# Kernel optimization log

Hardware: AMD Instinct MI355X
Metric: run time of the kernel (lower is better)

The kernel has to match this reference:

```python
import jax, jax.numpy as jnp
import numpy as np

EPS = 1e-5  # nn.GroupNorm default


def setup_inputs() -> dict:
    key = jax.random.key(0)
    k1, k2, k3 = jax.random.split(key, 3)
    N, B, C, H, W = 8, 4, 256, 64, 64
    blocks = jax.random.normal(k1, (N, B, C, H, W), dtype=jnp.float32)
    x = jax.random.normal(k2, (B, C, H, W), dtype=jnp.float32)
    w = jax.random.normal(k3, (C,), dtype=jnp.float32) * 0.02
    gn_weight = jnp.ones((C,), dtype=jnp.float32)
    gn_bias = jnp.zeros((C,), dtype=jnp.float32)
    return {"blocks": blocks, "x": x, "w": w, "gn_weight": gn_weight, "gn_bias": gn_bias}


def reference(blocks, x, w, gn_weight, gn_bias):
    # V: [N1, B, C, H, W] = prior blocks + current features
    V = jnp.concatenate([blocks, x[None]], axis=0)
    # GroupNorm(1, C): normalize over (C, H, W) per (n, b) sample, per-channel affine
    mean = jnp.mean(V, axis=(2, 3, 4), keepdims=True)
    var = jnp.var(V, axis=(2, 3, 4), keepdims=True)
    K = (V - mean) * jax.lax.rsqrt(var + EPS)
    K = K * gn_weight[None, None, :, None, None] + gn_bias[None, None, :, None, None]
    # channel-dim dot product -> logits over depth blocks
    logits = jnp.einsum('c,nbchw->nbhw', w, K)
    attn = jax.nn.softmax(logits, axis=0)  # softmax over depth-block axis N1
    h = jnp.einsum('nbhw,nbchw->bchw', attn, V)
    return h
```

## Files before the change

### kernel.cpp

```cpp
#include <hip/hip_runtime.h>


#define NPRI 8
#define N1   9
#define BB   4
#define CC   256
#define HWN  4096
#define CHW  (CC * HWN)
#define NB   (N1 * BB)
#define GN_EPS 1e-5f

#define WS_PSUM   0
#define WS_PSQ    2304
#define WS_SPART  4608
#define WS_ATTN   594432

__global__ __launch_bounds__(256, 4) void k1_stats(
        const float* __restrict__ blocks, const float* __restrict__ x,
        const float* __restrict__ w, const float* __restrict__ gnw,
        float* __restrict__ ws) {
    const int bid   = blockIdx.x;
    const int nb    = bid >> 6;
    const int rem   = bid & 63;
    const int cq    = rem >> 4;
    const int hwseg = rem & 15;
    const int t     = threadIdx.x;
    const int cg    = t >> 6;
    const int lane  = t & 63;

    const float* base = (nb < NPRI * BB)
        ? blocks + (size_t)nb * CHW
        : x + (size_t)(nb - NPRI * BB) * CHW;

    const int hw0 = hwseg * 256 + lane * 4;
    const int c0  = cq * 64 + cg * 16;

    float s0 = 0.f, s1 = 0.f, s2 = 0.f, s3 = 0.f;
    float sum = 0.f, sq = 0.f;

    #pragma unroll 4
    for (int c = c0; c < c0 + 16; ++c) {
        const float4 v = *reinterpret_cast<const float4*>(base + (size_t)c * HWN + hw0);
        const float wg = w[c] * gnw[c];
        sum += v.x + v.y + v.z + v.w;
        sq  += v.x * v.x + v.y * v.y + v.z * v.z + v.w * v.w;
        s0 += wg * v.x; s1 += wg * v.y; s2 += wg * v.z; s3 += wg * v.w;
    }

    __shared__ float4 sbuf[3][64];
    if (cg) sbuf[cg - 1][lane] = make_float4(s0, s1, s2, s3);
    __syncthreads();
    if (!cg) {
        #pragma unroll
        for (int g = 0; g < 3; ++g) {
            const float4 o = sbuf[g][lane];
            s0 += o.x; s1 += o.y; s2 += o.z; s3 += o.w;
        }
        float* Sp = ws + WS_SPART;
        *reinterpret_cast<float4*>(Sp + (size_t)(cq * NB + nb) * HWN + hw0) =
            make_float4(s0, s1, s2, s3);
    }

    #pragma unroll
    for (int off = 32; off; off >>= 1) {
        sum += __shfl_down(sum, off);
        sq  += __shfl_down(sq, off);
    }
    __shared__ float red[8];
    if (lane == 0) { red[cg] = sum; red[4 + cg] = sq; }
    __syncthreads();
    if (t == 0) {
        const int slot = nb * 64 + rem;
        ws[WS_PSUM + slot] = red[0] + red[1] + red[2] + red[3];
        ws[WS_PSQ  + slot] = red[4] + red[5] + red[6] + red[7];
    }
}

__global__ __launch_bounds__(256) void k2_attn(
        const float* __restrict__ w, const float* __restrict__ gnw,
        const float* __restrict__ gnb, float* __restrict__ ws) {
    const int t = threadIdx.x;

    __shared__ float red[8];
    __shared__ float swg_s, swgb_s;
    __shared__ float mean_s[NB], rstd_s[NB];

    float p = w[t] * gnw[t];
    float q = w[t] * gnb[t];
    #pragma unroll
    for (int off = 32; off; off >>= 1) {
        p += __shfl_down(p, off);
        q += __shfl_down(q, off);
    }
    const int wave = t >> 6, lane = t & 63;
    if (lane == 0) { red[wave] = p; red[4 + wave] = q; }

    if (t < NB) {
        float s = 0.f, ss = 0.f;
        #pragma unroll 8
        for (int i = 0; i < 64; ++i) {
            s  += ws[WS_PSUM + t * 64 + i];
            ss += ws[WS_PSQ  + t * 64 + i];
        }
        const float mean = s * (1.0f / CHW);
        const float var  = ss * (1.0f / CHW) - mean * mean;
        mean_s[t] = mean;
        rstd_s[t] = rsqrtf(var + GN_EPS);
    }
    __syncthreads();
    if (t == 0) {
        swg_s  = red[0] + red[1] + red[2] + red[3];
        swgb_s = red[4] + red[5] + red[6] + red[7];
    }
    __syncthreads();
    const float swg = swg_s, swgb = swgb_s;

    const int idx = blockIdx.x * 256 + t;
    const int b  = idx >> 12;
    const int hw = idx & 4095;

    const float* Sp = ws + WS_SPART;
    float* attn = ws + WS_ATTN;

    float logit[N1];
    float mx = -1e30f;
    #pragma unroll
    for (int n = 0; n < N1; ++n) {
        const int nb = n * BB + b;
        const size_t o = (size_t)nb * HWN + hw;
        const float S = Sp[o] + Sp[(size_t)NB * HWN + o]
                      + Sp[(size_t)2 * NB * HWN + o] + Sp[(size_t)3 * NB * HWN + o];
        const float l = rstd_s[nb] * (S - mean_s[nb] * swg) + swgb;
        logit[n] = l;
        mx = fmaxf(mx, l);
    }
    float denom = 0.f;
    #pragma unroll
    for (int n = 0; n < N1; ++n) {
        const float e = __expf(logit[n] - mx);
        logit[n] = e;
        denom += e;
    }
    const float inv = 1.0f / denom;
    #pragma unroll
    for (int n = 0; n < N1; ++n)
        attn[(size_t)(n * BB + b) * HWN + hw] = logit[n] * inv;
}

__global__ __launch_bounds__(256) void k3_out(
        const float* __restrict__ blocks, const float* __restrict__ x,
        const float* __restrict__ ws, float* __restrict__ out) {
    const int bid = blockIdx.x;
    const int hwq = bid & 3;
    const int c   = (bid >> 2) & (CC - 1);
    const int b   = bid >> 10;
    const int t   = threadIdx.x;
    const int hw0 = hwq * 1024 + t * 4;

    const float* attn = ws + WS_ATTN;
    float a0 = 0.f, a1 = 0.f, a2 = 0.f, a3 = 0.f;

    #pragma unroll
    for (int n = 0; n < N1; ++n) {
        const float* vbase = (n < NPRI)
            ? blocks + ((size_t)(n * BB + b) * CC + c) * HWN
            : x + ((size_t)b * CC + c) * HWN;
        const float4 v = *reinterpret_cast<const float4*>(vbase + hw0);
        const float4 a = *reinterpret_cast<const float4*>(
            attn + (size_t)(n * BB + b) * HWN + hw0);
        a0 += a.x * v.x; a1 += a.y * v.y; a2 += a.z * v.z; a3 += a.w * v.w;
    }
    float* optr = out + ((size_t)(b * CC + c)) * HWN + hw0;
    __builtin_nontemporal_store(a0, optr + 0);
    __builtin_nontemporal_store(a1, optr + 1);
    __builtin_nontemporal_store(a2, optr + 2);
    __builtin_nontemporal_store(a3, optr + 3);
}

extern "C" void kernel_launch(void* const* d_in, const int* in_sizes, int n_in,
                              void* d_out, int out_size, void* d_ws, size_t ws_size,
                              hipStream_t stream) {
    const float* blocks = (const float*)d_in[0];
    const float* x      = (const float*)d_in[1];
    const float* w      = (const float*)d_in[2];
    const float* gnw    = (const float*)d_in[3];
    const float* gnb    = (const float*)d_in[4];
    float* out = (float*)d_out;
    float* ws  = (float*)d_ws;

    hipLaunchKernelGGL(k1_stats, dim3(2304), dim3(256), 0, stream, blocks, x, w, gnw, ws);
    hipLaunchKernelGGL(k2_attn, dim3(64), dim3(256), 0, stream, w, gnw, gnb, ws);
    hipLaunchKernelGGL(k3_out, dim3(4096), dim3(256), 0, stream, blocks, x, ws, out);
}
```

Baseline: 59.42 us.

## Fuse softmax attention computation into output weighted-sum kernel

```diff
diff --git a/kernel.cpp b/kernel.cpp
--- a/kernel.cpp
+++ b/kernel.cpp
@@ -13,7 +13,6 @@
 #define WS_PSUM   0
 #define WS_PSQ    2304
 #define WS_SPART  4608
-#define WS_ATTN   594432
 
 __global__ __launch_bounds__(256, 4) void k1_stats(
         const float* __restrict__ blocks, const float* __restrict__ x,
@@ -76,24 +75,33 @@
     }
 }
 
-__global__ __launch_bounds__(256) void k2_attn(
+__global__ __launch_bounds__(256, 4) void k2_fused(
+        const float* __restrict__ blocks, const float* __restrict__ x,
         const float* __restrict__ w, const float* __restrict__ gnw,
-        const float* __restrict__ gnb, float* __restrict__ ws) {
-    const int t = threadIdx.x;
+        const float* __restrict__ gnb,
+        const float* __restrict__ ws, float* __restrict__ out) {
+    const int bid = blockIdx.x;
+    const int b   = bid >> 9;
+    const int hw0 = (bid & 511) * 8;
+    const int t   = threadIdx.x;
 
     __shared__ float red[8];
     __shared__ float swg_s, swgb_s;
     __shared__ float mean_s[NB], rstd_s[NB];
+    __shared__ float logit_s[N1][8];
+    __shared__ float4 attn4_s[N1][2];
 
-    float p = w[t] * gnw[t];
-    float q = w[t] * gnb[t];
-    #pragma unroll
-    for (int off = 32; off; off >>= 1) {
-        p += __shfl_down(p, off);
-        q += __shfl_down(q, off);
+    {
+        float p = w[t] * gnw[t];
+        float q = w[t] * gnb[t];
+        #pragma unroll
+        for (int off = 32; off; off >>= 1) {
+            p += __shfl_down(p, off);
+            q += __shfl_down(q, off);
+        }
+        const int wave = t >> 6, lane = t & 63;
+        if (lane == 0) { red[wave] = p; red[4 + wave] = q; }
     }
-    const int wave = t >> 6, lane = t & 63;
-    if (lane == 0) { red[wave] = p; red[4 + wave] = q; }
 
     if (t < NB) {
         float s = 0.f, ss = 0.f;
@@ -113,68 +121,63 @@
         swgb_s = red[4] + red[5] + red[6] + red[7];
     }
     __syncthreads();
-    const float swg = swg_s, swgb = swgb_s;
 
-    const int idx = blockIdx.x * 256 + t;
-    const int b  = idx >> 12;
-    const int hw = idx & 4095;
-
-    const float* Sp = ws + WS_SPART;
-    float* attn = ws + WS_ATTN;
-
-    float logit[N1];
-    float mx = -1e30f;
-    #pragma unroll
-    for (int n = 0; n < N1; ++n) {
-        const int nb = n * BB + b;
-        const size_t o = (size_t)nb * HWN + hw;
+    if (t < N1 * 8) {
+        const int n   = t >> 3;
+        const int hwi = t & 7;
+        const int nb  = n * BB + b;
+        const float* Sp = ws + WS_SPART;
+        const size_t o = (size_t)nb * HWN + hw0 + hwi;
         const float S = Sp[o] + Sp[(size_t)NB * HWN + o]
                       + Sp[(size_t)2 * NB * HWN + o] + Sp[(size_t)3 * NB * HWN + o];
-        const float l = rstd_s[nb] * (S - mean_s[nb] * swg) + swgb;
-        logit[n] = l;
-        mx = fmaxf(mx, l);
+        logit_s[n][hwi] = rstd_s[nb] * (S - mean_s[nb] * swg_s) + swgb_s;
     }
-    float denom = 0.f;
-    #pragma unroll
-    for (int n = 0; n < N1; ++n) {
-        const float e = __expf(logit[n] - mx);
-        logit[n] = e;
-        denom += e;
+    __syncthreads();
+
+    if (t < 8) {
+        float mx = -1e30f;
+        #pragma unroll
+        for (int n = 0; n < N1; ++n) mx = fmaxf(mx, logit_s[n][t]);
+        float den = 0.f;
+        float e[N1];
+        #pragma unroll
+        for (int n = 0; n < N1; ++n) { e[n] = __expf(logit_s[n][t] - mx); den += e[n]; }
+        const float inv = 1.0f / den;
+        float* attn_f = (float*)attn4_s;
+        #pragma unroll
+        for (int n = 0; n < N1; ++n) attn_f[n * 8 + t] = e[n] * inv;
     }
-    const float inv = 1.0f / denom;
-    #pragma unroll
-    for (int n = 0; n < N1; ++n)
-        attn[(size_t)(n * BB + b) * HWN + hw] = logit[n] * inv;
-}
+    __syncthreads();
 
-__global__ __launch_bounds__(256) void k3_out(
-        const float* __restrict__ blocks, const float* __restrict__ x,
-        const float* __restrict__ ws, float* __restrict__ out) {
-    const int bid = blockIdx.x;
-    const int hwq = bid & 3;
-    const int c   = (bid >> 2) & (CC - 1);
-    const int b   = bid >> 10;
-    const int t   = threadIdx.x;
-    const int hw0 = hwq * 1024 + t * 4;
+    const int hw4 = t & 1;
+    const int c_  = t >> 1;
+    const int hw  = hw0 + hw4 * 4;
 
-    const float* attn = ws + WS_ATTN;
-    float a0 = 0.f, a1 = 0.f, a2 = 0.f, a3 = 0.f;
+    float4 acc0 = make_float4(0.f, 0.f, 0.f, 0.f);
+    float4 acc1 = make_float4(0.f, 0.f, 0.f, 0.f);
 
     #pragma unroll
     for (int n = 0; n < N1; ++n) {
-        const float* vbase = (n < NPRI)
-            ? blocks + ((size_t)(n * BB + b) * CC + c) * HWN
-            : x + ((size_t)b * CC + c) * HWN;
-        const float4 v = *reinterpret_cast<const float4*>(vbase + hw0);
-        const float4 a = *reinterpret_cast<const float4*>(
-            attn + (size_t)(n * BB + b) * HWN + hw0);
-        a0 += a.x * v.x; a1 += a.y * v.y; a2 += a.z * v.z; a3 += a.w * v.w;
+        const float* vb = (n < NPRI)
+            ? blocks + (size_t)(n * BB + b) * CHW
+            : x + (size_t)b * CHW;
+        const float4 a  = attn4_s[n][hw4];
+        const float4 v0 = *reinterpret_cast<const float4*>(vb + (size_t)c_ * HWN + hw);
+        const float4 v1 = *reinterpret_cast<const float4*>(vb + (size_t)(c_ + 128) * HWN + hw);
+        acc0.x += a.x * v0.x; acc0.y += a.y * v0.y; acc0.z += a.z * v0.z; acc0.w += a.w * v0.w;
+        acc1.x += a.x * v1.x; acc1.y += a.y * v1.y; acc1.z += a.z * v1.z; acc1.w += a.w * v1.w;
     }
-    float* optr = out + ((size_t)(b * CC + c)) * HWN + hw0;
-    __builtin_nontemporal_store(a0, optr + 0);
-    __builtin_nontemporal_store(a1, optr + 1);
-    __builtin_nontemporal_store(a2, optr + 2);
-    __builtin_nontemporal_store(a3, optr + 3);
+
+    float* o0 = out + (size_t)(b * CC + c_) * HWN + hw;
+    float* o1 = out + (size_t)(b * CC + c_ + 128) * HWN + hw;
+    __builtin_nontemporal_store(acc0.x, o0 + 0);
+    __builtin_nontemporal_store(acc0.y, o0 + 1);
+    __builtin_nontemporal_store(acc0.z, o0 + 2);
+    __builtin_nontemporal_store(acc0.w, o0 + 3);
+    __builtin_nontemporal_store(acc1.x, o1 + 0);
+    __builtin_nontemporal_store(acc1.y, o1 + 1);
+    __builtin_nontemporal_store(acc1.z, o1 + 2);
+    __builtin_nontemporal_store(acc1.w, o1 + 3);
 }
 
 extern "C" void kernel_launch(void* const* d_in, const int* in_sizes, int n_in,
@@ -189,6 +192,6 @@
     float* ws  = (float*)d_ws;
 
     hipLaunchKernelGGL(k1_stats, dim3(2304), dim3(256), 0, stream, blocks, x, w, gnw, ws);
-    hipLaunchKernelGGL(k2_attn, dim3(64), dim3(256), 0, stream, w, gnw, gnb, ws);
-    hipLaunchKernelGGL(k3_out, dim3(4096), dim3(256), 0, stream, blocks, x, ws, out);
+    hipLaunchKernelGGL(k2_fused, dim3(2048), dim3(256), 0, stream,
+                       blocks, x, w, gnw, gnb, ws, out);
 }
```

Result: slower. 128.6 us (+116.5%).
